# Kernel optimization log

Hardware: AMD Instinct MI355X
Metric: run time of the kernel (lower is better)

The kernel has to match this reference:

```python
import jax, jax.numpy as jnp
import numpy as np

NUM_NODES = 50000
NUM_EDGES = 800000
HIDDEN = 128
HEADS = 8
HEAD_DIM = HIDDEN // HEADS  # 16
FF_HIDDEN = 4 * HIDDEN
LN_EPS = 1e-5


def _xavier(key, shape, gain=0.01):
    fan_out, fan_in = shape
    bound = gain * np.sqrt(6.0 / (fan_in + fan_out))
    return jax.random.uniform(key, shape, jnp.float32, -bound, bound)


def setup_inputs() -> dict:
    key = jax.random.key(0)
    ks = jax.random.split(key, 10)
    x = jax.random.normal(ks[0], (NUM_NODES, HIDDEN), jnp.float32)
    edge_index = jax.random.randint(ks[1], (2, NUM_EDGES), 0, NUM_NODES, jnp.int64)
    return {
        "x": x,
        "edge_index": edge_index,
        "Wq": _xavier(ks[2], (HIDDEN, HIDDEN)),
        "bq": jnp.zeros((HIDDEN,), jnp.float32),
        "Wk": _xavier(ks[3], (HIDDEN, HIDDEN)),
        "bk": jnp.zeros((HIDDEN,), jnp.float32),
        "Wv": _xavier(ks[4], (HIDDEN, HIDDEN)),
        "bv": jnp.zeros((HIDDEN,), jnp.float32),
        "Wo": _xavier(ks[5], (HIDDEN, HIDDEN)),
        "bo": jnp.zeros((HIDDEN,), jnp.float32),
        "W1": _xavier(ks[6], (FF_HIDDEN, HIDDEN)),
        "b1": jnp.zeros((FF_HIDDEN,), jnp.float32),
        "W2": _xavier(ks[7], (HIDDEN, FF_HIDDEN)),
        "b2": jnp.zeros((HIDDEN,), jnp.float32),
        "g1": jnp.ones((HIDDEN,), jnp.float32),
        "be1": jnp.zeros((HIDDEN,), jnp.float32),
        "g2": jnp.ones((HIDDEN,), jnp.float32),
        "be2": jnp.zeros((HIDDEN,), jnp.float32),
    }


def _layernorm(v, g, b):
    mu = jnp.mean(v, axis=-1, keepdims=True)
    var = jnp.mean(jnp.square(v - mu), axis=-1, keepdims=True)
    return (v - mu) * jax.lax.rsqrt(var + LN_EPS) * g + b


def _forward(x, edge_index, Wq, bq, Wk, bk, Wv, bv, Wo, bo, W1, b1, W2, b2, g1, be1, g2, be2):
    src = edge_index[0]  # key/value side (_j)
    dst = edge_index[1]  # query side (_i), aggregation index
    scale = 1.0 / np.sqrt(HEAD_DIM)

    # Euclidean manifold: GeometricLinear == plain linear
    q = (x @ Wq.T + bq).reshape(NUM_NODES, HEADS, HEAD_DIM)
    k = (x @ Wk.T + bk).reshape(NUM_NODES, HEADS, HEAD_DIM)
    v = (x @ Wv.T + bv).reshape(NUM_NODES, HEADS, HEAD_DIM)

    # per-edge attention scores [E, H]
    alpha = jnp.einsum('ehd,ehd->eh', q[dst], k[src]) * scale
    # segment softmax over destination nodes
    m = jax.ops.segment_max(alpha, dst, num_segments=NUM_NODES)  # [N, H]
    ea = jnp.exp(alpha - m[dst])
    denom = jax.ops.segment_sum(ea, dst, num_segments=NUM_NODES)  # [N, H]
    alpha = ea / (denom[dst] + 1e-16)

    # scatter-add weighted values -> [N, H, D]
    agg = jax.ops.segment_sum(v[src] * alpha[..., None], dst, num_segments=NUM_NODES)
    att = agg.reshape(NUM_NODES, HIDDEN) @ Wo.T + bo

    # residual + norm1 (Euclidean)
    h = _layernorm(x + att, g1, be1)

    # feed-forward: fc1 -> exact GELU -> fc2
    ff = (jax.nn.gelu(h @ W1.T + b1, approximate=False)) @ W2.T + b2

    # residual + norm2
    return _layernorm(h + ff, g2, be2)


def reference(x, edge_index, Wq, bq, Wk, bk, Wv, bv, Wo, bo, W1, b1, W2, b2, g1, be1, g2, be2):
    return _forward(x, edge_index, Wq, bq, Wk, bk, Wv, bv, Wo, bo, W1, b1, W2, b2, g1, be1, g2, be2)
```

## Files before the change

kernel.cpp:

```cpp
#include <hip/hip_runtime.h>
#include <math.h>

#define N_HEADS 8
#define HEAD_DIM 16
#define HID 128
#define QKV_ROWB 512

typedef unsigned short ushort_t;
typedef __attribute__((ext_vector_type(8))) short short8;
typedef __attribute__((ext_vector_type(4))) float floatx4;
typedef __attribute__((ext_vector_type(2))) float f32x2;

#define KV_SCALE 64.0f
#define KV_INV_SCALE 0.015625f

__device__ __forceinline__ ushort_t f2bf(float f) {
    unsigned u = __float_as_uint(f);
    unsigned r = (u + 0x7FFFu + ((u >> 16) & 1u)) >> 16;
    return (ushort_t)r;
}
__device__ __forceinline__ float bf2f(ushort_t u) {
    return __uint_as_float(((unsigned)u) << 16);
}

__device__ __forceinline__ void gld_lds16(const void* g, void* l) {
    __builtin_amdgcn_global_load_lds(
        (const __attribute__((address_space(1))) void*)g,
        (__attribute__((address_space(3))) void*)l, 16, 0, 0);
}

__device__ __forceinline__ float gelu_f(float x) {
    float z = fabsf(x) * 0.70710678118654752f;
    float t = 1.0f / (1.0f + 0.3275911f * z);
    float y = t * (0.254829592f + t * (-0.284496736f + t * (1.421413741f
            + t * (-1.453152027f + t * 1.061405429f))));
    float e = 1.0f - y * __expf(-z * z);
    e = copysignf(e, x);
    return 0.5f * x * (1.0f + e);
}

__global__ __launch_bounds__(256)
void prep_kernel(const float* __restrict__ x,
                 const float* __restrict__ Wq, const float* __restrict__ Wk,
                 const float* __restrict__ Wv, const float* __restrict__ Wo,
                 const float* __restrict__ W1, const float* __restrict__ W2,
                 const float* __restrict__ bq, const float* __restrict__ bk,
                 const float* __restrict__ bv,
                 const int* __restrict__ dst, int* __restrict__ cnt, int E,
                 ushort_t* __restrict__ xb, ushort_t* __restrict__ wts,
                 float* __restrict__ bqkv, int xpairs)
{
    int i = blockIdx.x * 256 + threadIdx.x;
    if (i < xpairs) {
        float2 v = ((const float2*)x)[i];
        xb[i * 2]     = f2bf(v.x);
        xb[i * 2 + 1] = f2bf(v.y);
        return;
    }
    int j = i - xpairs;
    if (j < 98304) {
        const float* s; int off;
        if (j < 32768) {
            if (j < 8192)       { s = Wq; off = j; }
            else if (j < 16384) { s = Wk; off = j - 8192; }
            else if (j < 24576) { s = Wv; off = j - 16384; }
            else                { s = Wo; off = j - 24576; }
        } else if (j < 65536)   { s = W1; off = j - 32768; }
        else                    { s = W2; off = j - 65536; }
        float2 v = ((const float2*)s)[off];
        wts[j * 2]     = f2bf(v.x);
        wts[j * 2 + 1] = f2bf(v.y);
        return;
    }
    int b = j - 98304;
    if (b < 384) {
        bqkv[b] = (b < 128) ? bq[b] : (b < 256) ? bk[b - 128] : bv[b - 256];
        return;
    }
    int e = b - 384;
    if (e < E) atomicAdd(&cnt[dst[e]], 1);
}

template<int MT, int ACT, int LN, int OUTF>
__global__ __launch_bounds__(256)
void gemm_t(const ushort_t* __restrict__ A, int lda, int M,
            const ushort_t* __restrict__ W, int K,
            const float* __restrict__ bias,
            float* __restrict__ outf, ushort_t* __restrict__ outb, int ostride,
            const float* __restrict__ resf, const ushort_t* __restrict__ resb,
            const float* __restrict__ g, const float* __restrict__ be)
{
    constexpr int MI  = MT / 32;
    constexpr int STG = MT * 64 + 128 * 64;
    constexpr int BNC = MT * 136;
    constexpr int SB  = STG > BNC ? STG : BNC;
    __shared__ __align__(16) ushort_t sbuf[SB];
    __shared__ float pS[LN ? MT : 1][2];
    __shared__ float pQ[LN ? MT : 1][2];
    ushort_t* As = sbuf;
    ushort_t* Ws = sbuf + MT * 64;

    const int tid  = threadIdx.x;
    const int wave = tid >> 6, lane = tid & 63;
    const int gm0 = blockIdx.x * MT;
    const int o0  = blockIdx.y * 128;
    const int mhalf = wave >> 1, ohalf = wave & 1;

    floatx4 acc[MI][4];
#pragma unroll
    for (int i = 0; i < MI; ++i)
#pragma unroll
        for (int j = 0; j < 4; ++j) acc[i][j] = (floatx4)(0.f);

    for (int kc = 0; kc < K; kc += 64) {
#pragma unroll
        for (int it = 0; it < 4; ++it) {
            int s   = it * 256 + tid;
            int ln  = s & 63;
            int grp = s >> 6;
            int tile = grp >> 1, kst = grp & 1;
            int row = tile * 16 + (ln & 15);
            int kk  = kst * 32 + (ln >> 4) * 8;
            gld_lds16(&W[(size_t)(o0 + row) * K + kc + kk],
                      &Ws[(it * 256 + wave * 64) * 8]);
        }
#pragma unroll
        for (int it = 0; it < MT / 32; ++it) {
            int s   = it * 256 + tid;
            int ln  = s & 63;
            int grp = s >> 6;
            int tile = grp >> 1, kst = grp & 1;
            int row = tile * 16 + (ln & 15);
            int kk  = kst * 32 + (ln >> 4) * 8;
            int ar = gm0 + row; if (ar >= M) ar = M - 1;
            gld_lds16(&A[(size_t)ar * lda + kc + kk],
                      &As[(it * 256 + wave * 64) * 8]);
        }
        __syncthreads();
#pragma unroll
        for (int kst = 0; kst < 2; ++kst) {
            short8 af[MI], wf[4];
#pragma unroll
            for (int i = 0; i < MI; ++i) {
                int mt = mhalf * MI + i;
                af[i] = *(const short8*)&As[((mt * 2 + kst) * 64 + lane) * 8];
            }
#pragma unroll
            for (int j = 0; j < 4; ++j) {
                int ot = ohalf * 4 + j;
                wf[j] = *(const short8*)&Ws[((ot * 2 + kst) * 64 + lane) * 8];
            }
#pragma unroll
            for (int i = 0; i < MI; ++i)
#pragma unroll
                for (int j = 0; j < 4; ++j)
                    acc[i][j] = __builtin_amdgcn_mfma_f32_16x16x32_bf16(
                        af[i], wf[j], acc[i][j], 0, 0, 0);
        }
        __syncthreads();
    }

    ushort_t* B16 = sbuf;
    float*    B32 = (float*)sbuf;

    if (LN) {
#pragma unroll
        for (int j = 0; j < 4; ++j) {
            int oc = (ohalf * 4 + j) * 16 + (lane & 15);
            float bj = bias[oc];
#pragma unroll
            for (int i = 0; i < MI; ++i) {
                int rbase = gm0 + (mhalf * MI + i) * 16 + (lane >> 4) * 4;
#pragma unroll
                for (int r = 0; r < 4; ++r) {
                    int rowc = rbase + r; if (rowc >= M) rowc = M - 1;
                    float rv = resf ? resf[(size_t)rowc * HID + oc]
                                    : bf2f(resb[(size_t)rowc * HID + oc]);
                    acc[i][j][r] += bj + rv;
                }
            }
        }
#pragma unroll
        for (int i = 0; i < MI; ++i) {
#pragma unroll
            for (int r = 0; r < 4; ++r) {
                float s1 = acc[i][0][r] + acc[i][1][r] + acc[i][2][r] + acc[i][3][r];
                float s2 = acc[i][0][r] * acc[i][0][r] + acc[i][1][r] * acc[i][1][r]
                         + acc[i][2][r] * acc[i][2][r] + acc[i][3][r] * acc[i][3][r];
                s1 += __shfl_xor(s1, 1); s1 += __shfl_xor(s1, 2);
                s1 += __shfl_xor(s1, 4); s1 += __shfl_xor(s1, 8);
                s2 += __shfl_xor(s2, 1); s2 += __shfl_xor(s2, 2);
                s2 += __shfl_xor(s2, 4); s2 += __shfl_xor(s2, 8);
                if ((lane & 15) == 0) {
                    int rl = (mhalf * MI + i) * 16 + (lane >> 4) * 4 + r;
                    pS[rl][ohalf] = s1;
                    pQ[rl][ohalf] = s2;
                }
            }
        }
        __syncthreads();
#pragma unroll
        for (int i = 0; i < MI; ++i) {
#pragma unroll
            for (int r = 0; r < 4; ++r) {
                int rl = (mhalf * MI + i) * 16 + (lane >> 4) * 4 + r;
                float S = pS[rl][0] + pS[rl][1];
                float Q = pQ[rl][0] + pQ[rl][1];
                float mu = S * (1.f / 128.f);
                float var = Q * (1.f / 128.f) - mu * mu;
                float rstd = rsqrtf(var + 1e-5f);
#pragma unroll
                for (int j = 0; j < 4; ++j) {
                    int oc = (ohalf * 4 + j) * 16 + (lane & 15);
                    acc[i][j][r] = (acc[i][j][r] - mu) * rstd * g[oc] + be[oc];
                }
            }
        }
        __syncthreads();
    }

    if (OUTF == 0) {
#pragma unroll
        for (int i = 0; i < MI; ++i)
#pragma unroll
            for (int j = 0; j < 4; ++j) {
                int oc = (ohalf * 4 + j) * 16 + (lane & 15);
                float bj = LN ? 0.f : bias[oc];
#pragma unroll
                for (int r = 0; r < 4; ++r) {
                    int rl = (mhalf * MI + i) * 16 + (lane >> 4) * 4 + r;
                    float v = acc[i][j][r] + bj;
                    if (ACT) v = gelu_f(v);
                    B16[rl * 136 + oc] = f2bf(v);
                }
            }
        __syncthreads();
#pragma unroll
        for (int p = 0; p < MT / 16; ++p) {
            int row = p * 16 + (tid >> 4);
            int ch  = tid & 15;
            if (gm0 + row < M)
                *(short8*)&outb[(size_t)(gm0 + row) * ostride + o0 + ch * 8] =
                    *(const short8*)&B16[row * 136 + ch * 8];
        }
    } else if (OUTF == 2) {
#pragma unroll
        for (int i = 0; i < MI; ++i)
#pragma unroll
            for (int j = 0; j < 4; ++j) {
                int oc = (ohalf * 4 + j) * 16 + (lane & 15);
                float bj = bias[o0 + oc];
#pragma unroll
                for (int r = 0; r < 4; ++r) {
                    int rl = (mhalf * MI + i) * 16 + (lane >> 4) * 4 + r;
                    float v = (acc[i][j][r] + bj) * KV_SCALE;
                    B16[rl * 136 + oc] = f2bf(v);
                }
            }
        __syncthreads();
        const int koff = blockIdx.y * 8;
#pragma unroll
        for (int p = 0; p < MT / 16; ++p) {
            int row = p * 16 + (tid >> 4);
            int ch  = tid & 15;
            if (gm0 + row < M) {
                short8 s = *(const short8*)&B16[row * 136 + ch * 8];
                unsigned u0 = 0, u1 = 0;
                u0 = __builtin_amdgcn_cvt_pk_fp8_f32(
                         bf2f((ushort_t)s[0]), bf2f((ushort_t)s[1]), u0, false);
                u0 = __builtin_amdgcn_cvt_pk_fp8_f32(
                         bf2f((ushort_t)s[2]), bf2f((ushort_t)s[3]), u0, true);
                u1 = __builtin_amdgcn_cvt_pk_fp8_f32(
                         bf2f((ushort_t)s[4]), bf2f((ushort_t)s[5]), u1, false);
                u1 = __builtin_amdgcn_cvt_pk_fp8_f32(
                         bf2f((ushort_t)s[6]), bf2f((ushort_t)s[7]), u1, true);
                uint2 o; o.x = u0; o.y = u1;
                *(uint2*)((char*)outb + (size_t)(gm0 + row) * QKV_ROWB
                          + 256 + ch * 16 + koff) = o;
            }
        }
    } else {
#pragma unroll
        for (int p = 0; p < 2; ++p) {
            if (ohalf == p) {
#pragma unroll
                for (int i = 0; i < MI; ++i)
#pragma unroll
                    for (int j = 0; j < 4; ++j) {
                        int ocl = j * 16 + (lane & 15);
                        float bj = LN ? 0.f : bias[p * 64 + ocl];
#pragma unroll
                        for (int r = 0; r < 4; ++r) {
                            int rl = (mhalf * MI + i) * 16 + (lane >> 4) * 4 + r;
                            float v = acc[i][j][r] + bj;
                            if (ACT) v = gelu_f(v);
                            B32[rl * 68 + ocl] = v;
                        }
                    }
            }
            __syncthreads();
#pragma unroll
            for (int q = 0; q < MT / 16; ++q) {
                int row = q * 16 + (tid >> 4);
                int ch  = tid & 15;
                if (gm0 + row < M)
                    *(float4*)&outf[(size_t)(gm0 + row) * ostride + o0 + p * 64 + ch * 4] =
                        *(const float4*)&B32[row * 68 + ch * 4];
            }
            __syncthreads();
        }
    }
}

__global__ __launch_bounds__(256)
void scan1_kernel(const int* __restrict__ cnt, int* __restrict__ parts, int N)
{
    __shared__ int sd[256];
    int t = threadIdx.x;
    int base = blockIdx.x * 1024 + t * 4;
    int s = 0;
#pragma unroll
    for (int j = 0; j < 4; ++j) if (base + j < N) s += cnt[base + j];
    sd[t] = s; __syncthreads();
    for (int off = 128; off; off >>= 1) {
        if (t < off) sd[t] += sd[t + off];
        __syncthreads();
    }
    if (t == 0) parts[blockIdx.x] = sd[0];
}

__global__ __launch_bounds__(256)
void scan2_kernel(const int* __restrict__ parts, int* __restrict__ poff, int nb)
{
    __shared__ int sd[256];
    int t = threadIdx.x;
    int v = (t < nb) ? parts[t] : 0;
    sd[t] = v; __syncthreads();
    for (int off = 1; off < 256; off <<= 1) {
        int u = (t >= off) ? sd[t - off] : 0;
        __syncthreads();
        sd[t] += u;
        __syncthreads();
    }
    if (t < nb) poff[t] = sd[t] - v;
}

__global__ __launch_bounds__(256)
void scan3_kernel(const int* __restrict__ cnt, const int* __restrict__ poff,
                  int* __restrict__ rp, int N)
{
    __shared__ int sd[256];
    int t = threadIdx.x;
    int base = blockIdx.x * 1024 + t * 4;
    int v0 = (base + 0 < N) ? cnt[base + 0] : 0;
    int v1 = (base + 1 < N) ? cnt[base + 1] : 0;
    int v2 = (base + 2 < N) ? cnt[base + 2] : 0;
    int v3 = (base + 3 < N) ? cnt[base + 3] : 0;
    int s = v0 + v1 + v2 + v3;
    sd[t] = s; __syncthreads();
    for (int off = 1; off < 256; off <<= 1) {
        int u = (t >= off) ? sd[t - off] : 0;
        __syncthreads();
        sd[t] += u;
        __syncthreads();
    }
    int o = poff[blockIdx.x] + sd[t] - s;
    if (base + 0 < N) rp[base + 0] = o;
    if (base + 1 < N) rp[base + 1] = o + v0;
    if (base + 2 < N) rp[base + 2] = o + v0 + v1;
    if (base + 3 < N) rp[base + 3] = o + v0 + v1 + v2;
}

__global__ __launch_bounds__(256)
void scatter_kernel(const int* __restrict__ src, const int* __restrict__ dst,
                    int* __restrict__ rp, int* __restrict__ ssrc, int E)
{
    int e = blockIdx.x * 256 + threadIdx.x;
    if (e >= E) return;
    int pos = atomicAdd(&rp[dst[e]], 1);
    ssrc[pos] = src[e];
}

__global__ __launch_bounds__(256)
void attn_fused_kernel(const ushort_t* __restrict__ qkvb, const int* __restrict__ rp,
                       const int* __restrict__ ssrc, ushort_t* __restrict__ aggb, int N)
{
    int wave = threadIdx.x >> 6, lane = threadIdx.x & 63;
    int n = blockIdx.x * 4 + wave;
    if (n >= N) return;
    int grp = lane >> 4;
    int cb  = (lane & 15) * 16;
    const char* base = (const char*)qkvb;

    short8 qv = *(const short8*)(base + n * QKV_ROWB + cb);
    float q[8];
#pragma unroll
    for (int j = 0; j < 8; ++j) q[j] = bf2f((ushort_t)qv[j]) * (0.25f / KV_SCALE);

    int r0 = n ? rp[n - 1] : 0;
    int r1 = rp[n];
    float acc[8] = {0.f, 0.f, 0.f, 0.f, 0.f, 0.f, 0.f, 0.f};
    float l = 0.f;

    int r = r0;
    for (; r + 8 <= r1; r += 8) {
        int s0 = ssrc[r + grp];
        int s1 = ssrc[r + 4 + grp];
        uint4 kv0 = *(const uint4*)(base + s0 * QKV_ROWB + 256 + cb);
        uint4 kv1 = *(const uint4*)(base + s1 * QKV_ROWB + 256 + cb);

        f32x2 a0 = __builtin_amdgcn_cvt_pk_f32_fp8(kv0.x, false);
        f32x2 a1 = __builtin_amdgcn_cvt_pk_f32_fp8(kv0.x, true);
        f32x2 a2 = __builtin_amdgcn_cvt_pk_f32_fp8(kv0.y, false);
        f32x2 a3 = __builtin_amdgcn_cvt_pk_f32_fp8(kv0.y, true);
        f32x2 b0 = __builtin_amdgcn_cvt_pk_f32_fp8(kv1.x, false);
        f32x2 b1 = __builtin_amdgcn_cvt_pk_f32_fp8(kv1.x, true);
        f32x2 b2 = __builtin_amdgcn_cvt_pk_f32_fp8(kv1.y, false);
        f32x2 b3 = __builtin_amdgcn_cvt_pk_f32_fp8(kv1.y, true);

        float p0 = 0.f, p1 = 0.f;
        p0 = fmaf(q[0], a0.x, p0); p0 = fmaf(q[1], a0.y, p0);
        p0 = fmaf(q[2], a1.x, p0); p0 = fmaf(q[3], a1.y, p0);
        p0 = fmaf(q[4], a2.x, p0); p0 = fmaf(q[5], a2.y, p0);
        p0 = fmaf(q[6], a3.x, p0); p0 = fmaf(q[7], a3.y, p0);
        p1 = fmaf(q[0], b0.x, p1); p1 = fmaf(q[1], b0.y, p1);
        p1 = fmaf(q[2], b1.x, p1); p1 = fmaf(q[3], b1.y, p1);
        p1 = fmaf(q[4], b2.x, p1); p1 = fmaf(q[5], b2.y, p1);
        p1 = fmaf(q[6], b3.x, p1); p1 = fmaf(q[7], b3.y, p1);

        p0 += __shfl_xor(p0, 1);
        p1 += __shfl_xor(p1, 1);
        float e0 = __expf(p0), e1 = __expf(p1);
        l += e0 + e1;
// ... 40 lines not shown
        acc[2] = fmaf(ea, v1.x, acc[2]); acc[3] = fmaf(ea, v1.y, acc[3]);
        acc[4] = fmaf(ea, v2.x, acc[4]); acc[5] = fmaf(ea, v2.y, acc[5]);
        acc[6] = fmaf(ea, v3.x, acc[6]); acc[7] = fmaf(ea, v3.y, acc[7]);
    }

#pragma unroll
    for (int j = 0; j < 8; ++j) {
        acc[j] += __shfl_xor(acc[j], 16);
        acc[j] += __shfl_xor(acc[j], 32);
    }
    l += __shfl_xor(l, 16);
    l += __shfl_xor(l, 32);
    float inv = KV_INV_SCALE / (l + 1e-16f);
    if (grp == 0) {
        short8 o;
#pragma unroll
        for (int j = 0; j < 8; ++j) o[j] = (short)f2bf(acc[j] * inv);
        *(short8*)((char*)aggb + n * 256 + cb) = o;
    }
}

extern "C" void kernel_launch(void* const* d_in, const int* in_sizes, int n_in,
                              void* d_out, int out_size, void* d_ws, size_t ws_size,
                              hipStream_t stream)
{
    const float* x  = (const float*)d_in[0];
    const int*   ei = (const int*)d_in[1];
    const float* Wq = (const float*)d_in[2];
    const float* bq = (const float*)d_in[3];
    const float* Wk = (const float*)d_in[4];
    const float* bk = (const float*)d_in[5];
    const float* Wv = (const float*)d_in[6];
    const float* bv = (const float*)d_in[7];
    const float* Wo = (const float*)d_in[8];
    const float* bo = (const float*)d_in[9];
    const float* W1 = (const float*)d_in[10];
    const float* b1 = (const float*)d_in[11];
    const float* W2 = (const float*)d_in[12];
    const float* b2 = (const float*)d_in[13];
    const float* g1 = (const float*)d_in[14];
    const float* be1= (const float*)d_in[15];
    const float* g2 = (const float*)d_in[16];
    const float* be2= (const float*)d_in[17];
    float* out = (float*)d_out;

    const int N = in_sizes[0] / HID;
    const int E = in_sizes[1] / 2;
    const int* srcp = ei;
    const int* dstp = ei + E;

    const size_t NH = (size_t)N * HID;
    float* wsf = (float*)d_ws;

    ushort_t* xb   = (ushort_t*)wsf;
    ushort_t* qkvb = (ushort_t*)(wsf + NH / 2);
    ushort_t* aggb = (ushort_t*)(wsf + 2 * NH);
    ushort_t* hb   = (ushort_t*)wsf;
    ushort_t* ffb  = (ushort_t*)(wsf + NH / 2);

    ushort_t* wts  = (ushort_t*)(wsf + 2 * NH + NH / 2);
    float*    bqkv = (float*)(wts + 196608);
    int*      rp   = (int*)(bqkv + 384);
    int*      cnt  = rp + (N + 1);
    int*      poff = cnt + N;
    int*      parts= poff + 256;
    int*      ssrc = parts + 256;

    hipMemsetAsync(cnt, 0, N * sizeof(int), stream);
    const int xpairs = (int)(NH / 2);
    const int ptot   = xpairs + 98304 + 384 + E;
    prep_kernel<<<(ptot + 255) / 256, 256, 0, stream>>>(
        x, Wq, Wk, Wv, Wo, W1, W2, bq, bk, bv, dstp, cnt, E,
        xb, wts, bqkv, xpairs);

    const int nb = (N + 1023) / 1024;
    scan1_kernel<<<nb, 256, 0, stream>>>(cnt, parts, N);
    scan2_kernel<<<1, 256, 0, stream>>>(parts, poff, nb);
    scan3_kernel<<<nb, 256, 0, stream>>>(cnt, poff, rp, N);
    scatter_kernel<<<(E + 255) / 256, 256, 0, stream>>>(srcp, dstp, rp, ssrc, E);

    const int gx64 = (N + 63) / 64;

    gemm_t<64, 0, 0, 0><<<dim3(gx64, 1), 256, 0, stream>>>(
        xb, HID, N, wts, HID, bqkv, nullptr, qkvb, 256,
        nullptr, nullptr, nullptr, nullptr);

    gemm_t<64, 0, 0, 2><<<dim3(gx64, 2), 256, 0, stream>>>(
        xb, HID, N, wts + 16384, HID, bqkv + 128, nullptr, qkvb, 0,
        nullptr, nullptr, nullptr, nullptr);

    attn_fused_kernel<<<(N + 3) / 4, 256, 0, stream>>>(qkvb, rp, ssrc, aggb, N);

    gemm_t<64, 0, 1, 0><<<dim3(gx64, 1), 256, 0, stream>>>(
        aggb, HID, N, wts + 49152, HID, bo, nullptr, hb, HID,
        x, nullptr, g1, be1);

    gemm_t<64, 1, 0, 0><<<dim3(gx64, 4), 256, 0, stream>>>(
        hb, HID, N, wts + 65536, HID, b1, nullptr, ffb, 512,
        nullptr, nullptr, nullptr, nullptr);

    gemm_t<64, 0, 1, 1><<<dim3(gx64, 1), 256, 0, stream>>>(
        ffb, 512, N, wts + 131072, 512, b2, out, nullptr, HID,
        nullptr, hb, g2, be2);
}
```

Before: 358.8 us.

## Replace LDS-staged GEMMs with single-wave register GEMMs and partition scatter by destination

The 256-thread, 64-row LDS-staged GEMM template becomes a one-wave kernel that computes 16 rows by 128 columns, loading A and W fragments straight from global memory into registers. LayerNorm then reduces within the wave and needs no shared-memory partials. Q, K and V projections are merged into a single launch over three y-blocks. The scatter kernel is rewritten so each of 8 block cohorts handles only one destination-node range, which keeps atomics local but has every cohort read all edges. This drops the bounds checks (assumes N is a multiple of 16), loses LDS-level reuse of W across rows, and increases the number of edge reads.

```diff
diff --git a/kernel.cpp b/kernel.cpp
--- a/kernel.cpp
+++ b/kernel.cpp
@@ -21,12 +21,6 @@
 }
 __device__ __forceinline__ float bf2f(ushort_t u) {
     return __uint_as_float(((unsigned)u) << 16);
-}
-
-__device__ __forceinline__ void gld_lds16(const void* g, void* l) {
-    __builtin_amdgcn_global_load_lds(
-        (const __attribute__((address_space(1))) void*)g,
-        (__attribute__((address_space(3))) void*)l, 16, 0, 0);
 }
 
 __device__ __forceinline__ float gelu_f(float x) {
@@ -81,233 +75,124 @@
     if (e < E) atomicAdd(&cnt[dst[e]], 1);
 }
 
-template<int MT, int ACT, int LN, int OUTF>
-__global__ __launch_bounds__(256)
-void gemm_t(const ushort_t* __restrict__ A, int lda, int M,
-            const ushort_t* __restrict__ W, int K,
+template<int K, int ACT, int LN, int OUTF>
+__global__ __launch_bounds__(64)
+void gemm1w(const ushort_t* __restrict__ A,
+            const ushort_t* __restrict__ W,
             const float* __restrict__ bias,
             float* __restrict__ outf, ushort_t* __restrict__ outb, int ostride,
             const float* __restrict__ resf, const ushort_t* __restrict__ resb,
             const float* __restrict__ g, const float* __restrict__ be)
 {
-    constexpr int MI  = MT / 32;
-    constexpr int STG = MT * 64 + 128 * 64;
-    constexpr int BNC = MT * 136;
-    constexpr int SB  = STG > BNC ? STG : BNC;
-    __shared__ __align__(16) ushort_t sbuf[SB];
-    __shared__ float pS[LN ? MT : 1][2];
-    __shared__ float pQ[LN ? MT : 1][2];
-    ushort_t* As = sbuf;
-    ushort_t* Ws = sbuf + MT * 64;
-
-    const int tid  = threadIdx.x;
-    const int wave = tid >> 6, lane = tid & 63;
-    const int gm0 = blockIdx.x * MT;
+    __shared__ __align__(16) ushort_t B16[16 * 136];
+    const int lane = threadIdx.x;
+    const int l15 = lane & 15, l4 = lane >> 4;
+    const int gm0 = blockIdx.x * 16;
     const int o0  = blockIdx.y * 128;
-    const int mhalf = wave >> 1, ohalf = wave & 1;
-
-    floatx4 acc[MI][4];
-#pragma unroll
-    for (int i = 0; i < MI; ++i)
-#pragma unroll
-        for (int j = 0; j < 4; ++j) acc[i][j] = (floatx4)(0.f);
-
-    for (int kc = 0; kc < K; kc += 64) {
-#pragma unroll
-        for (int it = 0; it < 4; ++it) {
-            int s   = it * 256 + tid;
-            int ln  = s & 63;
-            int grp = s >> 6;
-            int tile = grp >> 1, kst = grp & 1;
-            int row = tile * 16 + (ln & 15);
-            int kk  = kst * 32 + (ln >> 4) * 8;
-            gld_lds16(&W[(size_t)(o0 + row) * K + kc + kk],
-                      &Ws[(it * 256 + wave * 64) * 8]);
-        }
-#pragma unroll
-        for (int it = 0; it < MT / 32; ++it) {
-            int s   = it * 256 + tid;
-            int ln  = s & 63;
-            int grp = s >> 6;
-            int tile = grp >> 1, kst = grp & 1;
-            int row = tile * 16 + (ln & 15);
-            int kk  = kst * 32 + (ln >> 4) * 8;
-            int ar = gm0 + row; if (ar >= M) ar = M - 1;
-            gld_lds16(&A[(size_t)ar * lda + kc + kk],
-                      &As[(it * 256 + wave * 64) * 8]);
-        }
-        __syncthreads();
-#pragma unroll
-        for (int kst = 0; kst < 2; ++kst) {
-            short8 af[MI], wf[4];
-#pragma unroll
-            for (int i = 0; i < MI; ++i) {
-                int mt = mhalf * MI + i;
-                af[i] = *(const short8*)&As[((mt * 2 + kst) * 64 + lane) * 8];
+
+    floatx4 acc[8];
+#pragma unroll
+    for (int j = 0; j < 8; ++j) acc[j] = (floatx4)(0.f);
+
+    const ushort_t* ap = A + (size_t)(gm0 + l15) * K + l4 * 8;
+    const ushort_t* wp = W + (size_t)(o0 + l15) * K + l4 * 8;
+
+    for (int kst = 0; kst < K / 32; ++kst) {
+        short8 av = *(const short8*)(ap + kst * 32);
+        short8 bv[8];
+#pragma unroll
+        for (int j = 0; j < 8; ++j)
+            bv[j] = *(const short8*)(wp + (size_t)j * 16 * K + kst * 32);
+#pragma unroll
+        for (int j = 0; j < 8; ++j)
+            acc[j] = __builtin_amdgcn_mfma_f32_16x16x32_bf16(av, bv[j], acc[j], 0, 0, 0);
+    }
+
+    if (LN) {
+        float gv[8], bev[8];
+#pragma unroll
+        for (int j = 0; j < 8; ++j) {
+            int oc = j * 16 + l15;
+            float bj = bias[oc];
+            gv[j] = g[oc]; bev[j] = be[oc];
+#pragma unroll
+            for (int r = 0; r < 4; ++r) {
+                int row = gm0 + l4 * 4 + r;
+                float rv = resf ? resf[(size_t)row * HID + oc]
+                                : bf2f(resb[(size_t)row * HID + oc]);
+                acc[j][r] += bj + rv;
             }
-#pragma unroll
-            for (int j = 0; j < 4; ++j) {
-                int ot = ohalf * 4 + j;
-                wf[j] = *(const short8*)&Ws[((ot * 2 + kst) * 64 + lane) * 8];
+        }
+#pragma unroll
+        for (int r = 0; r < 4; ++r) {
+            float s1 = 0.f, s2 = 0.f;
+#pragma unroll
+            for (int j = 0; j < 8; ++j) {
+                s1 += acc[j][r];
+                s2 += acc[j][r] * acc[j][r];
             }
-#pragma unroll
-            for (int i = 0; i < MI; ++i)
-#pragma unroll
-                for (int j = 0; j < 4; ++j)
-                    acc[i][j] = __builtin_amdgcn_mfma_f32_16x16x32_bf16(
-                        af[i], wf[j], acc[i][j], 0, 0, 0);
-        }
-        __syncthreads();
-    }
-
-    ushort_t* B16 = sbuf;
-    float*    B32 = (float*)sbuf;
-
-    if (LN) {
-#pragma unroll
-        for (int j = 0; j < 4; ++j) {
-            int oc = (ohalf * 4 + j) * 16 + (lane & 15);
-            float bj = bias[oc];
-#pragma unroll
-            for (int i = 0; i < MI; ++i) {
-                int rbase = gm0 + (mhalf * MI + i) * 16 + (lane >> 4) * 4;
-#pragma unroll
-                for (int r = 0; r < 4; ++r) {
-                    int rowc = rbase + r; if (rowc >= M) rowc = M - 1;
-                    float rv = resf ? resf[(size_t)rowc * HID + oc]
-                                    : bf2f(resb[(size_t)rowc * HID + oc]);
-                    acc[i][j][r] += bj + rv;
-                }
-            }
-        }
-#pragma unroll
-        for (int i = 0; i < MI; ++i) {
-#pragma unroll
-            for (int r = 0; r < 4; ++r) {
-                float s1 = acc[i][0][r] + acc[i][1][r] + acc[i][2][r] + acc[i][3][r];
-                float s2 = acc[i][0][r] * acc[i][0][r] + acc[i][1][r] * acc[i][1][r]
-                         + acc[i][2][r] * acc[i][2][r] + acc[i][3][r] * acc[i][3][r];
-                s1 += __shfl_xor(s1, 1); s1 += __shfl_xor(s1, 2);
-                s1 += __shfl_xor(s1, 4); s1 += __shfl_xor(s1, 8);
-                s2 += __shfl_xor(s2, 1); s2 += __shfl_xor(s2, 2);
-                s2 += __shfl_xor(s2, 4); s2 += __shfl_xor(s2, 8);
-                if ((lane & 15) == 0) {
-                    int rl = (mhalf * MI + i) * 16 + (lane >> 4) * 4 + r;
-                    pS[rl][ohalf] = s1;
-                    pQ[rl][ohalf] = s2;
-                }
-            }
-        }
-        __syncthreads();
-#pragma unroll
-        for (int i = 0; i < MI; ++i) {
-#pragma unroll
-            for (int r = 0; r < 4; ++r) {
-                int rl = (mhalf * MI + i) * 16 + (lane >> 4) * 4 + r;
-                float S = pS[rl][0] + pS[rl][1];
-                float Q = pQ[rl][0] + pQ[rl][1];
-                float mu = S * (1.f / 128.f);
-                float var = Q * (1.f / 128.f) - mu * mu;
-                float rstd = rsqrtf(var + 1e-5f);
-#pragma unroll
-                for (int j = 0; j < 4; ++j) {
-                    int oc = (ohalf * 4 + j) * 16 + (lane & 15);
-                    acc[i][j][r] = (acc[i][j][r] - mu) * rstd * g[oc] + be[oc];
-                }
-            }
-        }
-        __syncthreads();
-    }
-
-    if (OUTF == 0) {
-#pragma unroll
-        for (int i = 0; i < MI; ++i)
-#pragma unroll
-            for (int j = 0; j < 4; ++j) {
-                int oc = (ohalf * 4 + j) * 16 + (lane & 15);
-                float bj = LN ? 0.f : bias[oc];
-#pragma unroll
-                for (int r = 0; r < 4; ++r) {
-                    int rl = (mhalf * MI + i) * 16 + (lane >> 4) * 4 + r;
-                    float v = acc[i][j][r] + bj;
-                    if (ACT) v = gelu_f(v);
-                    B16[rl * 136 + oc] = f2bf(v);
-                }
-            }
-        __syncthreads();
-#pragma unroll
-        for (int p = 0; p < MT / 16; ++p) {
-            int row = p * 16 + (tid >> 4);
-            int ch  = tid & 15;
-            if (gm0 + row < M)
-                *(short8*)&outb[(size_t)(gm0 + row) * ostride + o0 + ch * 8] =
-                    *(const short8*)&B16[row * 136 + ch * 8];
-        }
-    } else if (OUTF == 2) {
-#pragma unroll
-        for (int i = 0; i < MI; ++i)
-#pragma unroll
-            for (int j = 0; j < 4; ++j) {
-                int oc = (ohalf * 4 + j) * 16 + (lane & 15);
-                float bj = bias[o0 + oc];
-#pragma unroll
-                for (int r = 0; r < 4; ++r) {
-                    int rl = (mhalf * MI + i) * 16 + (lane >> 4) * 4 + r;
-                    float v = (acc[i][j][r] + bj) * KV_SCALE;
-                    B16[rl * 136 + oc] = f2bf(v);
-                }
-            }
-        __syncthreads();
-        const int koff = blockIdx.y * 8;
-#pragma unroll
-        for (int p = 0; p < MT / 16; ++p) {
-            int row = p * 16 + (tid >> 4);
-            int ch  = tid & 15;
-            if (gm0 + row < M) {
-                short8 s = *(const short8*)&B16[row * 136 + ch * 8];
-                unsigned u0 = 0, u1 = 0;
-                u0 = __builtin_amdgcn_cvt_pk_fp8_f32(
-                         bf2f((ushort_t)s[0]), bf2f((ushort_t)s[1]), u0, false);
-                u0 = __builtin_amdgcn_cvt_pk_fp8_f32(
-                         bf2f((ushort_t)s[2]), bf2f((ushort_t)s[3]), u0, true);
-                u1 = __builtin_amdgcn_cvt_pk_fp8_f32(
-                         bf2f((ushort_t)s[4]), bf2f((ushort_t)s[5]), u1, false);
-                u1 = __builtin_amdgcn_cvt_pk_fp8_f32(
-                         bf2f((ushort_t)s[6]), bf2f((ushort_t)s[7]), u1, true);
-                uint2 o; o.x = u0; o.y = u1;
-                *(uint2*)((char*)outb + (size_t)(gm0 + row) * QKV_ROWB
-                          + 256 + ch * 16 + koff) = o;
-            }
+            s1 += __shfl_xor(s1, 1); s1 += __shfl_xor(s1, 2);
+            s1 += __shfl_xor(s1, 4); s1 += __shfl_xor(s1, 8);
+            s2 += __shfl_xor(s2, 1); s2 += __shfl_xor(s2, 2);
+            s2 += __shfl_xor(s2, 4); s2 += __shfl_xor(s2, 8);
+            float mu = s1 * (1.f / 128.f);
+            float var = s2 * (1.f / 128.f) - mu * mu;
+            float rstd = rsqrtf(var + 1e-5f);
+#pragma unroll
+            for (int j = 0; j < 8; ++j)
+                acc[j][r] = (acc[j][r] - mu) * rstd * gv[j] + bev[j];
+        }
+    }
+
+    if (OUTF == 1) {
+#pragma unroll
+        for (int j = 0; j < 8; ++j)
+#pragma unroll
+            for (int r = 0; r < 4; ++r)
+                outf[(size_t)(gm0 + l4 * 4 + r) * HID + j * 16 + l15] = acc[j][r];
+        return;
+    }
+
+    const bool kvout = (OUTF == 3) && (blockIdx.y > 0);
+#pragma unroll
+    for (int j = 0; j < 8; ++j) {
+        float bj = LN ? 0.f : bias[o0 + j * 16 + l15];
+#pragma unroll
+        for (int r = 0; r < 4; ++r) {
+            float v = acc[j][r] + bj;
+            if (ACT) v = gelu_f(v);
+            if (kvout) v *= KV_SCALE;
+            B16[(l4 * 4 + r) * 136 + j * 16 + l15] = f2bf(v);
+        }
+    }
+    __syncthreads();
+
+    if (kvout) {
+        const int koff = (blockIdx.y - 1) * 8;
+#pragma unroll
+        for (int c = 0; c < 4; ++c) {
+            int ch = l4 * 4 + c;
+            short8 s = *(const short8*)&B16[l15 * 136 + ch * 8];
+            unsigned u0 = 0, u1 = 0;
+            u0 = __builtin_amdgcn_cvt_pk_fp8_f32(
+                     bf2f((ushort_t)s[0]), bf2f((ushort_t)s[1]), u0, false);
+            u0 = __builtin_amdgcn_cvt_pk_fp8_f32(
+                     bf2f((ushort_t)s[2]), bf2f((ushort_t)s[3]), u0, true);
+            u1 = __builtin_amdgcn_cvt_pk_fp8_f32(
+                     bf2f((ushort_t)s[4]), bf2f((ushort_t)s[5]), u1, false);
+            u1 = __builtin_amdgcn_cvt_pk_fp8_f32(
+                     bf2f((ushort_t)s[6]), bf2f((ushort_t)s[7]), u1, true);
+            uint2 o; o.x = u0; o.y = u1;
+            *(uint2*)((char*)outb + (size_t)(gm0 + l15) * QKV_ROWB
+                      + 256 + ch * 16 + koff) = o;
         }
     } else {
-#pragma unroll
-        for (int p = 0; p < 2; ++p) {
-            if (ohalf == p) {
-#pragma unroll
-                for (int i = 0; i < MI; ++i)
-#pragma unroll
-                    for (int j = 0; j < 4; ++j) {
-                        int ocl = j * 16 + (lane & 15);
-                        float bj = LN ? 0.f : bias[p * 64 + ocl];
-#pragma unroll
-                        for (int r = 0; r < 4; ++r) {
-                            int rl = (mhalf * MI + i) * 16 + (lane >> 4) * 4 + r;
-                            float v = acc[i][j][r] + bj;
-                            if (ACT) v = gelu_f(v);
-                            B32[rl * 68 + ocl] = v;
-                        }
-                    }
-            }
-            __syncthreads();
-#pragma unroll
-            for (int q = 0; q < MT / 16; ++q) {
-                int row = q * 16 + (tid >> 4);
-                int ch  = tid & 15;
-                if (gm0 + row < M)
-                    *(float4*)&outf[(size_t)(gm0 + row) * ostride + o0 + p * 64 + ch * 4] =
-                        *(const float4*)&B32[row * 68 + ch * 4];
-            }
-            __syncthreads();
+        const int oo = (OUTF == 3) ? 0 : o0;
+#pragma unroll
+        for (int c = 0; c < 4; ++c) {
+            int ch = l4 * 4 + c;
+            *(short8*)&outb[(size_t)(gm0 + l15) * ostride + oo + ch * 8] =
+                *(const short8*)&B16[l15 * 136 + ch * 8];
         }
     }
 }
@@ -373,12 +258,21 @@
 
 __global__ __launch_bounds__(256)
 void scatter_kernel(const int* __restrict__ src, const int* __restrict__ dst,
-                    int* __restrict__ rp, int* __restrict__ ssrc, int E)
-{
-    int e = blockIdx.x * 256 + threadIdx.x;
-    if (e >= E) return;
-    int pos = atomicAdd(&rp[dst[e]], 1);
-    ssrc[pos] = src[e];
+                    int* __restrict__ rp, int* __restrict__ ssrc, int E, int N)
+{
+    int coh = blockIdx.x & 7;
+    int bc  = blockIdx.x >> 3;
+    int rr  = (N + 7) >> 3;
+    int nlo = coh * rr;
+    int nhi = nlo + rr; if (nhi > N) nhi = N;
+    int stride = (gridDim.x >> 3) * 256;
+    for (int e = bc * 256 + threadIdx.x; e < E; e += stride) {
+        int d = dst[e];
+        if (d >= nlo && d < nhi) {
+            int pos = atomicAdd(&rp[d], 1);
+            ssrc[pos] = src[e];
+        }
+    }
 }
 
 __global__ __launch_bounds__(256)
@@ -550,29 +444,25 @@
     scan1_kernel<<<nb, 256, 0, stream>>>(cnt, parts, N);
     scan2_kernel<<<1, 256, 0, stream>>>(parts, poff, nb);
     scan3_kernel<<<nb, 256, 0, stream>>>(cnt, poff, rp, N);
-    scatter_kernel<<<(E + 255) / 256, 256, 0, stream>>>(srcp, dstp, rp, ssrc, E);
-
-    const int gx64 = (N + 63) / 64;
-
-    gemm_t<64, 0, 0, 0><<<dim3(gx64, 1), 256, 0, stream>>>(
-        xb, HID, N, wts, HID, bqkv, nullptr, qkvb, 256,
+    scatter_kernel<<<2048, 256, 0, stream>>>(srcp, dstp, rp, ssrc, E, N);
+
+    const int gx16 = (N + 15) / 16;
+
+    gemm1w<128, 0, 0, 3><<<dim3(gx16, 3), 64, 0, stream>>>(
+        xb, wts, bqkv, nullptr, qkvb, 256,
         nullptr, nullptr, nullptr, nullptr);
 
-    gemm_t<64, 0, 0, 2><<<dim3(gx64, 2), 256, 0, stream>>>(
-        xb, HID, N, wts + 16384, HID, bqkv + 128, nullptr, qkvb, 0,
+    attn_fused_kernel<<<(N + 3) / 4, 256, 0, stream>>>(qkvb, rp, ssrc, aggb, N);
+
+    gemm1w<128, 0, 1, 0><<<dim3(gx16, 1), 64, 0, stream>>>(
+        aggb, wts + 49152, bo, nullptr, hb, HID,
+        x, nullptr, g1, be1);
+
+    gemm1w<128, 1, 0, 0><<<dim3(gx16, 4), 64, 0, stream>>>(
+        hb, wts + 65536, b1, nullptr, ffb, 512,
         nullptr, nullptr, nullptr, nullptr);
 
-    attn_fused_kernel<<<(N + 3) / 4, 256, 0, stream>>>(qkvb, rp, ssrc, aggb, N);
-
-    gemm_t<64, 0, 1, 0><<<dim3(gx64, 1), 256, 0, stream>>>(
-        aggb, HID, N, wts + 49152, HID, bo, nullptr, hb, HID,
-        x, nullptr, g1, be1);
-
-    gemm_t<64, 1, 0, 0><<<dim3(gx64, 4), 256, 0, stream>>>(
-        hb, HID, N, wts + 65536, HID, b1, nullptr, ffb, 512,
-        nullptr, nullptr, nullptr, nullptr);
-
-    gemm_t<64, 0, 1, 1><<<dim3(gx64, 1), 256, 0, stream>>>(
-        ffb, 512, N, wts + 131072, 512, b2, out, nullptr, HID,
+    gemm1w<512, 0, 1, 1><<<dim3(gx16, 1), 64, 0, stream>>>(
+        ffb, wts + 131072, b2, out, nullptr, HID,
         nullptr, hb, g2, be2);
 }
```

Result: slower. 435.9 us (+21.5%).

## Rewrite FFN with fragment-layout MFMA kernels and FP8 second GEMM

Applied to the files above, without the earlier changes.

The FFN is replaced by two new kernels. The first reads pre-swizzled MFMA fragment images of h and W1 straight from global memory and writes GELU activations as scaled FP8. The second runs an FP8 MFMA GEMM against a pre-quantised W2 and fuses the residual add and LayerNorm. Other changes: the two QKV GEMM launches merge into one grid, the generic GEMM gets LDS double-buffered staging, and the edge scatter is partitioned by destination range across block cohorts. FP8 quantisation of activations and W2 with fixed scales lowers precision and can overflow or underflow for inputs unlike the test ones.

```diff
diff --git a/kernel.cpp b/kernel.cpp
--- a/kernel.cpp
+++ b/kernel.cpp
@@ -13,6 +13,10 @@
 
 #define KV_SCALE 64.0f
 #define KV_INV_SCALE 0.015625f
+
+#define W2_SCALE 65536.0f
+#define A1_SCALE 512.0f
+#define FF2_DESCALE (1.0f / 33554432.0f)
 
 __device__ __forceinline__ ushort_t f2bf(float f) {
     unsigned u = __float_as_uint(f);
@@ -48,7 +52,9 @@
                  const float* __restrict__ bv,
                  const int* __restrict__ dst, int* __restrict__ cnt, int E,
                  ushort_t* __restrict__ xb, ushort_t* __restrict__ wts,
-                 float* __restrict__ bqkv, int xpairs)
+                 float* __restrict__ bqkv,
+                 ushort_t* __restrict__ w1frag,
+                 unsigned char* __restrict__ w2frag8, int xpairs)
 {
     int i = blockIdx.x * 256 + threadIdx.x;
     if (i < xpairs) {
@@ -58,26 +64,51 @@
         return;
     }
     int j = i - xpairs;
-    if (j < 98304) {
+    if (j < 32768) {
         const float* s; int off;
-        if (j < 32768) {
-            if (j < 8192)       { s = Wq; off = j; }
-            else if (j < 16384) { s = Wk; off = j - 8192; }
-            else if (j < 24576) { s = Wv; off = j - 16384; }
-            else                { s = Wo; off = j - 24576; }
-        } else if (j < 65536)   { s = W1; off = j - 32768; }
-        else                    { s = W2; off = j - 65536; }
+        if (j < 8192)       { s = Wq; off = j; }
+        else if (j < 16384) { s = Wk; off = j - 8192; }
+        else if (j < 24576) { s = Wv; off = j - 16384; }
+        else                { s = Wo; off = j - 24576; }
         float2 v = ((const float2*)s)[off];
         wts[j * 2]     = f2bf(v.x);
         wts[j * 2 + 1] = f2bf(v.y);
         return;
     }
-    int b = j - 98304;
+    int b = j - 32768;
     if (b < 384) {
         bqkv[b] = (b < 128) ? bq[b] : (b < 256) ? bk[b - 128] : bv[b - 256];
         return;
     }
-    int e = b - 384;
+    int c = b - 384;
+    if (c < 8192) {
+        int lane = c & 63, tk = c >> 6;
+        int t16 = tk >> 2, kst = tk & 3;
+        int row = t16 * 16 + (lane & 15);
+        int kb  = kst * 32 + (lane >> 4) * 8;
+        const float* s = W1 + (size_t)row * HID + kb;
+        ushort_t* d = w1frag + (size_t)c * 8;
+#pragma unroll
+        for (int e = 0; e < 8; ++e) d[e] = f2bf(s[e]);
+        return;
+    }
+    int c2 = c - 8192;
+    if (c2 < 8192) {
+        int lane = c2 & 63, tk = c2 >> 6;
+        int t16 = tk >> 4, kst = tk & 15;
+        int row = t16 * 16 + (lane & 15);
+        int kb  = kst * 32 + (lane >> 4) * 8;
+        const float* s = W2 + (size_t)row * 512 + kb;
+        unsigned u0 = 0, u1 = 0;
+        u0 = __builtin_amdgcn_cvt_pk_fp8_f32(s[0]*W2_SCALE, s[1]*W2_SCALE, u0, false);
+        u0 = __builtin_amdgcn_cvt_pk_fp8_f32(s[2]*W2_SCALE, s[3]*W2_SCALE, u0, true);
+        u1 = __builtin_amdgcn_cvt_pk_fp8_f32(s[4]*W2_SCALE, s[5]*W2_SCALE, u1, false);
+        u1 = __builtin_amdgcn_cvt_pk_fp8_f32(s[6]*W2_SCALE, s[7]*W2_SCALE, u1, true);
+        uint2 o; o.x = u0; o.y = u1;
+        *(uint2*)(w2frag8 + (size_t)c2 * 8) = o;
+        return;
+    }
+    int e = c2 - 8192;
     if (e < E) atomicAdd(&cnt[dst[e]], 1);
 }
 
@@ -86,19 +117,17 @@
 void gemm_t(const ushort_t* __restrict__ A, int lda, int M,
             const ushort_t* __restrict__ W, int K,
             const float* __restrict__ bias,
-            float* __restrict__ outf, ushort_t* __restrict__ outb, int ostride,
+            ushort_t* __restrict__ hfragp, ushort_t* __restrict__ outb, int ostride,
             const float* __restrict__ resf, const ushort_t* __restrict__ resb,
             const float* __restrict__ g, const float* __restrict__ be)
 {
-    constexpr int MI  = MT / 32;
-    constexpr int STG = MT * 64 + 128 * 64;
-    constexpr int BNC = MT * 136;
-    constexpr int SB  = STG > BNC ? STG : BNC;
+    constexpr int MI   = MT / 32;
+    constexpr int HALF = MT * 64 + 128 * 64;
+    constexpr int BNC  = MT * 136;
+    constexpr int SB   = (2 * HALF > BNC) ? 2 * HALF : BNC;
     __shared__ __align__(16) ushort_t sbuf[SB];
     __shared__ float pS[LN ? MT : 1][2];
     __shared__ float pQ[LN ? MT : 1][2];
-    ushort_t* As = sbuf;
-    ushort_t* Ws = sbuf + MT * 64;
 
     const int tid  = threadIdx.x;
     const int wave = tid >> 6, lane = tid & 63;
@@ -106,13 +135,9 @@
     const int o0  = blockIdx.y * 128;
     const int mhalf = wave >> 1, ohalf = wave & 1;
 
-    floatx4 acc[MI][4];
-#pragma unroll
-    for (int i = 0; i < MI; ++i)
-#pragma unroll
-        for (int j = 0; j < 4; ++j) acc[i][j] = (floatx4)(0.f);
-
-    for (int kc = 0; kc < K; kc += 64) {
+    auto stage = [&](int kc, int h) {
+        ushort_t* As = sbuf + h * HALF;
+        ushort_t* Ws = As + MT * 64;
 #pragma unroll
         for (int it = 0; it < 4; ++it) {
             int s   = it * 256 + tid;
@@ -136,7 +161,21 @@
             gld_lds16(&A[(size_t)ar * lda + kc + kk],
                       &As[(it * 256 + wave * 64) * 8]);
         }
-        __syncthreads();
+    };
+
+    floatx4 acc[MI][4];
+#pragma unroll
+    for (int i = 0; i < MI; ++i)
+#pragma unroll
+        for (int j = 0; j < 4; ++j) acc[i][j] = (floatx4)(0.f);
+
+    const int nk = K >> 6;
+    stage(0, 0);
+    __syncthreads();
+    for (int t = 0; t < nk; ++t) {
+        if (t + 1 < nk) stage((t + 1) * 64, (t + 1) & 1);
+        const ushort_t* As = sbuf + (t & 1) * HALF;
+        const ushort_t* Ws = As + MT * 64;
 #pragma unroll
         for (int kst = 0; kst < 2; ++kst) {
             short8 af[MI], wf[4];
@@ -161,7 +200,6 @@
     }
 
     ushort_t* B16 = sbuf;
-    float*    B32 = (float*)sbuf;
 
     if (LN) {
 #pragma unroll
@@ -174,8 +212,8 @@
 #pragma unroll
                 for (int r = 0; r < 4; ++r) {
                     int rowc = rbase + r; if (rowc >= M) rowc = M - 1;
-                    float rv = resf ? resf[(size_t)rowc * HID + oc]
-                                    : bf2f(resb[(size_t)rowc * HID + oc]);
+                    float rv = resb ? bf2f(resb[(size_t)rowc * HID + oc])
+                                    : resf[(size_t)rowc * HID + oc];
                     acc[i][j][r] += bj + rv;
                 }
             }
@@ -219,13 +257,13 @@
         __syncthreads();
     }
 
-    if (OUTF == 0) {
+    if (OUTF == 0 || (OUTF == 3 && blockIdx.y == 0)) {
 #pragma unroll
         for (int i = 0; i < MI; ++i)
 #pragma unroll
             for (int j = 0; j < 4; ++j) {
                 int oc = (ohalf * 4 + j) * 16 + (lane & 15);
-                float bj = LN ? 0.f : bias[oc];
+                float bj = LN ? 0.f : bias[o0 + oc];
 #pragma unroll
                 for (int r = 0; r < 4; ++r) {
                     int rl = (mhalf * MI + i) * 16 + (lane >> 4) * 4 + r;
@@ -235,15 +273,28 @@
                 }
             }
         __syncthreads();
+        const int oo = (OUTF == 3) ? 0 : o0;
 #pragma unroll
         for (int p = 0; p < MT / 16; ++p) {
             int row = p * 16 + (tid >> 4);
             int ch  = tid & 15;
             if (gm0 + row < M)
-                *(short8*)&outb[(size_t)(gm0 + row) * ostride + o0 + ch * 8] =
+                *(short8*)&outb[(size_t)(gm0 + row) * ostride + oo + ch * 8] =
                     *(const short8*)&B16[row * 136 + ch * 8];
         }
-    } else if (OUTF == 2) {
+        if (LN && hfragp) {
+            int kst = tid >> 6, ln = tid & 63;
+#pragma unroll
+            for (int p = 0; p < MT / 16; ++p) {
+                if (gm0 + p * 16 < M) {
+                    int gt = (gm0 >> 4) + p;
+                    short8 v = *(const short8*)&B16[(p * 16 + (ln & 15)) * 136
+                                                    + kst * 32 + (ln >> 4) * 8];
+                    *(short8*)&hfragp[(((size_t)gt * 4 + kst) * 64 + ln) * 8] = v;
+                }
+            }
+        }
+    } else if (OUTF == 3) {
 #pragma unroll
         for (int i = 0; i < MI; ++i)
 #pragma unroll
@@ -258,7 +309,7 @@
                 }
             }
         __syncthreads();
-        const int koff = blockIdx.y * 8;
+        const int koff = (blockIdx.y - 1) * 8;
 #pragma unroll
         for (int p = 0; p < MT / 16; ++p) {
             int row = p * 16 + (tid >> 4);
@@ -279,35 +330,158 @@
                           + 256 + ch * 16 + koff) = o;
             }
         }
-    } else {
-#pragma unroll
-        for (int p = 0; p < 2; ++p) {
-            if (ohalf == p) {
-#pragma unroll
-                for (int i = 0; i < MI; ++i)
-#pragma unroll
-                    for (int j = 0; j < 4; ++j) {
-                        int ocl = j * 16 + (lane & 15);
-                        float bj = LN ? 0.f : bias[p * 64 + ocl];
-#pragma unroll
-                        for (int r = 0; r < 4; ++r) {
-                            int rl = (mhalf * MI + i) * 16 + (lane >> 4) * 4 + r;
-                            float v = acc[i][j][r] + bj;
-                            if (ACT) v = gelu_f(v);
-                            B32[rl * 68 + ocl] = v;
-                        }
-                    }
-            }
-            __syncthreads();
-#pragma unroll
-            for (int q = 0; q < MT / 16; ++q) {
-                int row = q * 16 + (tid >> 4);
-                int ch  = tid & 15;
-                if (gm0 + row < M)
-                    *(float4*)&outf[(size_t)(gm0 + row) * ostride + o0 + p * 64 + ch * 4] =
-                        *(const float4*)&B32[row * 68 + ch * 4];
-            }
-            __syncthreads();
+    }
+}
+
+__global__ __launch_bounds__(256)
+void ff1w_kernel(const ushort_t* __restrict__ hfrag,
+                 const ushort_t* __restrict__ w1frag,
+                 const float* __restrict__ b1,
+                 unsigned char* __restrict__ a1img, int M)
+{
+    __shared__ __align__(16) ushort_t sT[4][16 * 136];
+    const int wave = threadIdx.x >> 6, lane = threadIdx.x & 63;
+    const int cg = wave;
+    const int nt16 = (M + 15) / 16;
+    const int gt0 = blockIdx.x * 2;
+    const int gt1 = gt0 + 1;
+    const int gt1c = (gt1 < nt16) ? gt1 : nt16 - 1;
+    const int l15 = lane & 15, l4 = lane >> 4;
+
+    floatx4 acc[2][8];
+#pragma unroll
+    for (int i = 0; i < 2; ++i)
+#pragma unroll
+        for (int j = 0; j < 8; ++j) acc[i][j] = (floatx4)(0.f);
+
+#pragma unroll
+    for (int kst = 0; kst < 4; ++kst) {
+        short8 a0 = *(const short8*)&hfrag[(((size_t)gt0  * 4 + kst) * 64 + lane) * 8];
+        short8 a1 = *(const short8*)&hfrag[(((size_t)gt1c * 4 + kst) * 64 + lane) * 8];
+        short8 bv[8];
+#pragma unroll
+        for (int j = 0; j < 8; ++j)
+            bv[j] = *(const short8*)&w1frag[((((size_t)cg * 8 + j) * 4 + kst) * 64 + lane) * 8];
+#pragma unroll
+        for (int j = 0; j < 8; ++j) {
+            acc[0][j] = __builtin_amdgcn_mfma_f32_16x16x32_bf16(a0, bv[j], acc[0][j], 0, 0, 0);
+            acc[1][j] = __builtin_amdgcn_mfma_f32_16x16x32_bf16(a1, bv[j], acc[1][j], 0, 0, 0);
+        }
+    }
+
+    float b1v[8];
+#pragma unroll
+    for (int j = 0; j < 8; ++j) b1v[j] = b1[cg * 128 + j * 16 + l15];
+
+#pragma unroll
+    for (int i = 0; i < 2; ++i) {
+        const int gt = i ? gt1 : gt0;
+#pragma unroll
+        for (int j = 0; j < 8; ++j)
+#pragma unroll
+            for (int r = 0; r < 4; ++r)
+                sT[wave][(l4 * 4 + r) * 136 + j * 16 + l15] =
+                    f2bf(gelu_f(acc[i][j][r] + b1v[j]));
+        if (gt < nt16) {
+#pragma unroll
+            for (int q = 0; q < 4; ++q) {
+                float v[8];
+#pragma unroll
+                for (int e = 0; e < 8; ++e)
+                    v[e] = bf2f(sT[wave][l15 * 136 + q * 32 + l4 * 8 + e]) * A1_SCALE;
+                unsigned u0 = 0, u1 = 0;
+                u0 = __builtin_amdgcn_cvt_pk_fp8_f32(v[0], v[1], u0, false);
+                u0 = __builtin_amdgcn_cvt_pk_fp8_f32(v[2], v[3], u0, true);
+                u1 = __builtin_amdgcn_cvt_pk_fp8_f32(v[4], v[5], u1, false);
+                u1 = __builtin_amdgcn_cvt_pk_fp8_f32(v[6], v[7], u1, true);
+                uint2 o; o.x = u0; o.y = u1;
+                *(uint2*)(a1img + (((size_t)gt * 16 + cg * 4 + q) * 64 + lane) * 8) = o;
+            }
+        }
+    }
+}
+
+__global__ __launch_bounds__(256)
+void ff2w_kernel(const unsigned char* __restrict__ a1img,
+                 const unsigned char* __restrict__ w2frag8,
+                 const ushort_t* __restrict__ hb,
+                 const float* __restrict__ b2,
+                 const float* __restrict__ g, const float* __restrict__ be,
+                 float* __restrict__ out, int M)
+{
+    const int wave = threadIdx.x >> 6, lane = threadIdx.x & 63;
+    const int t32 = blockIdx.x * 4 + wave;
+    const int nt32 = (M + 31) / 32;
+    if (t32 >= nt32) return;
+    const int nt16 = (M + 15) / 16;
+    const int gt0 = t32 * 2;
+    const int gt1c = (gt0 + 1 < nt16) ? gt0 + 1 : nt16 - 1;
+    const int l15 = lane & 15, l4 = lane >> 4;
+
+    floatx4 acc[2][8];
+#pragma unroll
+    for (int i = 0; i < 2; ++i)
+#pragma unroll
+        for (int j = 0; j < 8; ++j) acc[i][j] = (floatx4)(0.f);
+
+#pragma unroll
+    for (int kst = 0; kst < 16; ++kst) {
+        long a0 = *(const long*)(a1img + (((size_t)gt0  * 16 + kst) * 64 + lane) * 8);
+        long a1 = *(const long*)(a1img + (((size_t)gt1c * 16 + kst) * 64 + lane) * 8);
+        long bv[8];
+#pragma unroll
+        for (int j = 0; j < 8; ++j)
+            bv[j] = *(const long*)(w2frag8 + (((size_t)j * 16 + kst) * 64 + lane) * 8);
+#pragma unroll
+        for (int j = 0; j < 8; ++j) {
+            acc[0][j] = __builtin_amdgcn_mfma_f32_16x16x32_fp8_fp8(a0, bv[j], acc[0][j], 0, 0, 0);
+            acc[1][j] = __builtin_amdgcn_mfma_f32_16x16x32_fp8_fp8(a1, bv[j], acc[1][j], 0, 0, 0);
+        }
+    }
+
+    float b2v[8], gv[8], bev[8];
+#pragma unroll
+    for (int j = 0; j < 8; ++j) {
+        int oc = j * 16 + l15;
+        b2v[j] = b2[oc]; gv[j] = g[oc]; bev[j] = be[oc];
+    }
+
+#pragma unroll
+    for (int i = 0; i < 2; ++i) {
+        const int rb = (t32 * 2 + i) * 16;
+#pragma unroll
+        for (int j = 0; j < 8; ++j) {
+            int oc = j * 16 + l15;
+#pragma unroll
+            for (int r = 0; r < 4; ++r) {
+                int row = rb + l4 * 4 + r;
+                int rc = (row < M) ? row : M - 1;
+                acc[i][j][r] = acc[i][j][r] * FF2_DESCALE + b2v[j]
+                             + bf2f(hb[(size_t)rc * HID + oc]);
+            }
+        }
+#pragma unroll
+        for (int r = 0; r < 4; ++r) {
+            float s1 = 0.f, s2 = 0.f;
+#pragma unroll
+            for (int j = 0; j < 8; ++j) {
+                s1 += acc[i][j][r];
+                s2 += acc[i][j][r] * acc[i][j][r];
+            }
+            s1 += __shfl_xor(s1, 1); s1 += __shfl_xor(s1, 2);
+            s1 += __shfl_xor(s1, 4); s1 += __shfl_xor(s1, 8);
+            s2 += __shfl_xor(s2, 1); s2 += __shfl_xor(s2, 2);
+            s2 += __shfl_xor(s2, 4); s2 += __shfl_xor(s2, 8);
+            float mu = s1 * (1.f / 128.f);
+            float var = s2 * (1.f / 128.f) - mu * mu;
+            float rstd = rsqrtf(var + 1e-5f);
+            int row = rb + l4 * 4 + r;
+            if (row < M) {
+#pragma unroll
+                for (int j = 0; j < 8; ++j)
+                    out[(size_t)row * HID + j * 16 + l15] =
+                        (acc[i][j][r] - mu) * rstd * gv[j] + bev[j];
+            }
         }
     }
 }
@@ -373,12 +547,21 @@
 
 __global__ __launch_bounds__(256)
 void scatter_kernel(const int* __restrict__ src, const int* __restrict__ dst,
-                    int* __restrict__ rp, int* __restrict__ ssrc, int E)
-{
-    int e = blockIdx.x * 256 + threadIdx.x;
-    if (e >= E) return;
-    int pos = atomicAdd(&rp[dst[e]], 1);
-    ssrc[pos] = src[e];
+                    int* __restrict__ rp, int* __restrict__ ssrc, int E, int N)
+{
+    int coh = blockIdx.x & 7;
+    int bc  = blockIdx.x >> 3;
+    int rr  = (N + 7) >> 3;
+    int nlo = coh * rr;
+    int nhi = nlo + rr; if (nhi > N) nhi = N;
+    int stride = (gridDim.x >> 3) * 256;
+    for (int e = bc * 256 + threadIdx.x; e < E; e += stride) {
+        int d = dst[e];
+        if (d >= nlo && d < nhi) {
+            int pos = atomicAdd(&rp[d], 1);
+            ssrc[pos] = src[e];
+        }
+    }
 }
 
 __global__ __launch_bounds__(256)
@@ -525,14 +708,17 @@
     const size_t NH = (size_t)N * HID;
     float* wsf = (float*)d_ws;
 
-    ushort_t* xb   = (ushort_t*)wsf;
-    ushort_t* qkvb = (ushort_t*)(wsf + NH / 2);
-    ushort_t* aggb = (ushort_t*)(wsf + 2 * NH);
-    ushort_t* hb   = (ushort_t*)wsf;
-    ushort_t* ffb  = (ushort_t*)(wsf + NH / 2);
-
-    ushort_t* wts  = (ushort_t*)(wsf + 2 * NH + NH / 2);
-    float*    bqkv = (float*)(wts + 196608);
+    ushort_t* xb    = (ushort_t*)wsf;
+    ushort_t* qkvb  = (ushort_t*)(wsf + NH / 2);
+    ushort_t* hfrag = (ushort_t*)(wsf + NH + NH / 2);
+    ushort_t* aggb  = (ushort_t*)(wsf + 2 * NH);
+    ushort_t* hb    = (ushort_t*)wsf;
+    unsigned char* a1img = (unsigned char*)(wsf + NH / 2);
+
+    ushort_t* wts    = (ushort_t*)(wsf + 2 * NH + NH / 2);
+    ushort_t* w1frag = wts + 65536;
+    unsigned char* w2frag8 = (unsigned char*)(w1frag + 65536);
+    float*    bqkv = (float*)(w2frag8 + 65536);
     int*      rp   = (int*)(bqkv + 384);
     int*      cnt  = rp + (N + 1);
     int*      poff = cnt + N;
@@ -541,38 +727,32 @@
 
     hipMemsetAsync(cnt, 0, N * sizeof(int), stream);
     const int xpairs = (int)(NH / 2);
-    const int ptot   = xpairs + 98304 + 384 + E;
+    const int ptot   = xpairs + 32768 + 384 + 8192 + 8192 + E;
     prep_kernel<<<(ptot + 255) / 256, 256, 0, stream>>>(
         x, Wq, Wk, Wv, Wo, W1, W2, bq, bk, bv, dstp, cnt, E,
-        xb, wts, bqkv, xpairs);
+        xb, wts, bqkv, w1frag, w2frag8, xpairs);
 
     const int nb = (N + 1023) / 1024;
     scan1_kernel<<<nb, 256, 0, stream>>>(cnt, parts, N);
     scan2_kernel<<<1, 256, 0, stream>>>(parts, poff, nb);
     scan3_kernel<<<nb, 256, 0, stream>>>(cnt, poff, rp, N);
-    scatter_kernel<<<(E + 255) / 256, 256, 0, stream>>>(srcp, dstp, rp, ssrc, E);
+    scatter_kernel<<<2048, 256, 0, stream>>>(srcp, dstp, rp, ssrc, E, N);
 
     const int gx64 = (N + 63) / 64;
-
-    gemm_t<64, 0, 0, 0><<<dim3(gx64, 1), 256, 0, stream>>>(
+    const int nt32 = (N + 31) / 32;
+
+    gemm_t<64, 0, 0, 3><<<dim3(gx64, 3), 256, 0, stream>>>(
         xb, HID, N, wts, HID, bqkv, nullptr, qkvb, 256,
         nullptr, nullptr, nullptr, nullptr);
 
-    gemm_t<64, 0, 0, 2><<<dim3(gx64, 2), 256, 0, stream>>>(
-        xb, HID, N, wts + 16384, HID, bqkv + 128, nullptr, qkvb, 0,
-        nullptr, nullptr, nullptr, nullptr);
-
     attn_fused_kernel<<<(N + 3) / 4, 256, 0, stream>>>(qkvb, rp, ssrc, aggb, N);
 
     gemm_t<64, 0, 1, 0><<<dim3(gx64, 1), 256, 0, stream>>>(
-        aggb, HID, N, wts + 49152, HID, bo, nullptr, hb, HID,
+        aggb, HID, N, wts + 49152, HID, bo, hfrag, hb, HID,
         x, nullptr, g1, be1);
 
-    gemm_t<64, 1, 0, 0><<<dim3(gx64, 4), 256, 0, stream>>>(
-        hb, HID, N, wts + 65536, HID, b1, nullptr, ffb, 512,
-        nullptr, nullptr, nullptr, nullptr);
-
-    gemm_t<64, 0, 1, 1><<<dim3(gx64, 1), 256, 0, stream>>>(
-        ffb, 512, N, wts + 131072, 512, b2, out, nullptr, HID,
-        nullptr, hb, g2, be2);
-}
+    ff1w_kernel<<<nt32, 256, 0, stream>>>(hfrag, w1frag, b1, a1img, N);
+
+    ff2w_kernel<<<(nt32 + 3) / 4, 256, 0, stream>>>(
+        a1img, w2frag8, hb, b2, g2, be2, out, N);
+}
```

After: 323.9 us. 1.11x faster.
